# Optimization experiments

Measured on AMD Instinct MI355X. Metric: run time of the kernel, lower is better.

Reference implementation:

```python
import jax, jax.numpy as jnp
import numpy as np

B, H, W, C = 16, 128, 128, 256
C8 = C // 8


def setup_inputs() -> dict:
    key = jax.random.key(0)
    ks = jax.random.split(key, 7)
    s = 0.02
    return {
        "x": jax.random.normal(ks[0], (B, H, W, C), dtype=jnp.float32),
        "wq": jax.random.normal(ks[1], (C, C8), dtype=jnp.float32) * s,
        "bq": jnp.zeros((C8,), dtype=jnp.float32),
        "wk": jax.random.normal(ks[2], (C, C8), dtype=jnp.float32) * s,
        "bk": jnp.zeros((C8,), dtype=jnp.float32),
        "wv": jax.random.normal(ks[3], (C, C), dtype=jnp.float32) * s,
        "bv": jnp.zeros((C,), dtype=jnp.float32),
    }


def reference(x, wq, bq, wk, bk, wv, bv):
    # 1x1 convs == per-pixel linear projections
    q = jnp.einsum("bhwc,cd->bhwd", x, wq) + bq  # [B,H,W,C/8]
    k = jnp.einsum("bhwc,cd->bhwd", x, wk) + bk  # [B,H,W,C/8]
    v = jnp.einsum("bhwc,cd->bhwd", x, wv) + bv  # [B,H,W,C]
    # tf.matmul on 4D: batch over (B,H), attention over W (row-wise)
    scores = jnp.einsum("bhwd,bhvd->bhwv", q, k)  # [B,H,W,W]
    attn = jax.nn.softmax(scores, axis=-1)
    out = jnp.einsum("bhwv,bhvc->bhwc", attn, v)  # [B,H,W,C]
    return out
```

## Files before the change

### kernel.cpp

```cpp
#include <hip/hip_runtime.h>

typedef __attribute__((ext_vector_type(8))) short short8;
typedef __attribute__((ext_vector_type(16))) float f32x16;
typedef __attribute__((ext_vector_type(4))) float float4v;
typedef __attribute__((ext_vector_type(4))) unsigned short ushort4v;
typedef unsigned short u16;

#define MFMA32(a, b, c) __builtin_amdgcn_mfma_f32_32x32x16_bf16((a), (b), (c), 0, 0, 0)

#define W_ 128
#define C_ 256
#define X_LD 136
#define VT_LD 136
#define QK_LD 40
#define P_LD 136

__device__ __forceinline__ u16 f2bf(float f) {
    unsigned u = __builtin_bit_cast(unsigned, f);
    u += 0x7fffu + ((u >> 16) & 1u);
    return (u16)(u >> 16);
}

__device__ __forceinline__ f32x16 zero16() {
    f32x16 z;
#pragma unroll
    for (int i = 0; i < 16; ++i) z[i] = 0.f;
    return z;
}

__device__ __forceinline__ void gll16(const u16* g, const u16* l) {
    auto s = (const __attribute__((address_space(1))) unsigned*)((uintptr_t)g);
    auto d = (__attribute__((address_space(3))) unsigned*)((unsigned)(uintptr_t)l);
    __builtin_amdgcn_global_load_lds(s, d, 16, 0, 0);
}

__device__ __forceinline__ void wg_barrier() {
    asm volatile("s_waitcnt lgkmcnt(0)" ::: "memory");
    __builtin_amdgcn_sched_barrier(0);
    __builtin_amdgcn_s_barrier();
}

__global__ __launch_bounds__(256) void prep_pack(const float* __restrict__ wq,
                                                 const float* __restrict__ wk,
                                                 const float* __restrict__ wv,
                                                 u16* __restrict__ pack) {
    int t = blockIdx.x * 256 + threadIdx.x;
    int j = t & 7;
    int l = (t >> 3) & 63;
    int g = t >> 9;
    int f = g % 10;
    int ktg = g / 10;
    int k = ktg * 16 + ((l >> 5) << 3) + j;
    int c = l & 31;
    float w;
    if (f == 0)      w = wq[k * 32 + c];
    else if (f == 1) w = wk[k * 32 + c];
    else             w = wv[k * 256 + (f - 2) * 32 + c];
    pack[t] = f2bf(w);
}

__global__ __launch_bounds__(256, 2) void attn_fused(
        const float* __restrict__ x,
        const u16* __restrict__ pack,
        const float* __restrict__ bq, const float* __restrict__ bk,
        const float* __restrict__ bv,
        float* __restrict__ out) {
    __shared__ u16 uA[17408];
    __shared__ u16 uC[17408];

    const int slice = blockIdx.x;
    const int tid = threadIdx.x;
    const int lane = tid & 63;
    const int wid = tid >> 6;
    const int lm = lane & 31;
    const int l5 = lane >> 5;
    const int rowbase = wid * 32;
    const float* xs = x + (size_t)slice * (W_ * C_);

    const u16* vw0 = pack + (size_t)(2 + wid) * 512 + lane * 8;
    const u16* vw1 = pack + (size_t)(2 + wid + 4) * 512 + lane * 8;

    f32x16 qa = zero16();
    f32x16 ka = zero16();
    f32x16 vac0[4], vac1[4];
#pragma unroll
    for (int nn = 0; nn < 4; ++nn) { vac0[nn] = zero16(); vac1[nn] = zero16(); }

#pragma unroll
    for (int i = 0; i < 4; ++i) {
        int ks = wid * 4 + i;
        const u16* gs = pack + (size_t)ks * 5120 + lane * 8;
        gll16(gs, &uC[(ks * 2 + 0) * 512]);
        gll16(gs + 512, &uC[(ks * 2 + 1) * 512]);
    }

    for (int c = 0; c < 2; ++c) {
        if (c == 1) wg_barrier();
        {
            int r0 = tid >> 5;
            int col = (tid & 31) * 4;
#pragma unroll
            for (int p = 0; p < 16; ++p) {
                int row = p * 8 + r0;
                float4v xv = *reinterpret_cast<const float4v*>(xs + row * C_ + c * 128 + col);
                ushort4v b4;
                b4[0] = f2bf(xv[0]); b4[1] = f2bf(xv[1]);
                b4[2] = f2bf(xv[2]); b4[3] = f2bf(xv[3]);
                *reinterpret_cast<ushort4v*>(&uA[row * X_LD + col]) = b4;
            }
        }
        __syncthreads();

        short8 wf0[4], wf1[4];
        wf0[0] = *reinterpret_cast<const short8*>(vw0 + (size_t)(c * 8 + 0) * 5120);
        wf1[0] = *reinterpret_cast<const short8*>(vw1 + (size_t)(c * 8 + 0) * 5120);
        wf0[1] = *reinterpret_cast<const short8*>(vw0 + (size_t)(c * 8 + 1) * 5120);
        wf1[1] = *reinterpret_cast<const short8*>(vw1 + (size_t)(c * 8 + 1) * 5120);

#pragma unroll
        for (int kt = 0; kt < 8; ++kt) {
            const int ks = c * 8 + kt;
            if (kt < 6) {
                wf0[(kt + 2) & 3] = *reinterpret_cast<const short8*>(vw0 + (size_t)(ks + 2) * 5120);
                wf1[(kt + 2) & 3] = *reinterpret_cast<const short8*>(vw1 + (size_t)(ks + 2) * 5120);
            }
            short8 xf[4];
#pragma unroll
            for (int nn = 0; nn < 4; ++nn)
                xf[nn] = *reinterpret_cast<const short8*>(&uA[(nn * 32 + lm) * X_LD + kt * 16 + l5 * 8]);
            short8 aqk = *reinterpret_cast<const short8*>(&uA[(rowbase + lm) * X_LD + kt * 16 + l5 * 8]);
            short8 bq8 = *reinterpret_cast<const short8*>(&uC[(ks * 2 + 0) * 512 + lane * 8]);
            short8 bk8 = *reinterpret_cast<const short8*>(&uC[(ks * 2 + 1) * 512 + lane * 8]);
            qa = MFMA32(aqk, bq8, qa);
            ka = MFMA32(aqk, bk8, ka);
#pragma unroll
            for (int nn = 0; nn < 4; ++nn) {
                vac0[nn] = MFMA32(wf0[kt & 3], xf[nn], vac0[nn]);
                vac1[nn] = MFMA32(wf1[kt & 3], xf[nn], vac1[nn]);
            }
        }
    }
    wg_barrier();

    {
        float bqv = bq[lm];
        float bkv = bk[lm];
#pragma unroll
        for (int e = 0; e < 16; ++e) {
            int row = rowbase + (e & 3) + 8 * (e >> 2) + 4 * l5;
            uC[row * QK_LD + lm] = f2bf(qa[e] + bqv);
            uC[5120 + row * QK_LD + lm] = f2bf(ka[e] + bkv);
        }
    }
#pragma unroll
    for (int e = 0; e < 16; ++e) {
        int cl = (e & 3) + 8 * (e >> 2) + 4 * l5;
        float bvv = bv[wid * 32 + cl];
#pragma unroll
        for (int nn = 0; nn < 4; ++nn)
            uA[(wid * 32 + cl) * VT_LD + nn * 32 + lm] = f2bf(vac0[nn][e] + bvv);
    }
    wg_barrier();

    f32x16 s[4];
#pragma unroll
    for (int c2 = 0; c2 < 4; ++c2) s[c2] = zero16();
#pragma unroll
    for (int kt = 0; kt < 2; ++kt) {
        short8 aq = *reinterpret_cast<const short8*>(&uC[(rowbase + lm) * QK_LD + kt * 16 + l5 * 8]);
#pragma unroll
        for (int c2 = 0; c2 < 4; ++c2) {
            short8 bkf = *reinterpret_cast<const short8*>(&uC[5120 + (c2 * 32 + lm) * QK_LD + kt * 16 + l5 * 8]);
            s[c2] = MFMA32(aq, bkf, s[c2]);
        }
    }
    wg_barrier();

#pragma unroll
    for (int e = 0; e < 16; ++e) {
        float m = fmaxf(fmaxf(s[0][e], s[1][e]), fmaxf(s[2][e], s[3][e]));
        m = fmaxf(m, __shfl_xor(m, 1));
        m = fmaxf(m, __shfl_xor(m, 2));
        m = fmaxf(m, __shfl_xor(m, 4));
        m = fmaxf(m, __shfl_xor(m, 8));
        m = fmaxf(m, __shfl_xor(m, 16));
        float e0 = __expf(s[0][e] - m);
        float e1 = __expf(s[1][e] - m);
        float e2 = __expf(s[2][e] - m);
        float e3 = __expf(s[3][e] - m);
        float sum = (e0 + e1) + (e2 + e3);
        sum += __shfl_xor(sum, 1);
        sum += __shfl_xor(sum, 2);
        sum += __shfl_xor(sum, 4);
        sum += __shfl_xor(sum, 8);
        sum += __shfl_xor(sum, 16);
        float inv = 1.0f / sum;
        int row = rowbase + (e & 3) + 8 * (e >> 2) + 4 * l5;
        uC[row * P_LD + lm] = f2bf(e0 * inv);
        uC[row * P_LD + 32 + lm] = f2bf(e1 * inv);
        uC[row * P_LD + 64 + lm] = f2bf(e2 * inv);
        uC[row * P_LD + 96 + lm] = f2bf(e3 * inv);
    }

    float* os = out + (size_t)slice * (W_ * C_);

    f32x16 oc[4];
#pragma unroll
    for (int c2 = 0; c2 < 4; ++c2) oc[c2] = zero16();
#pragma unroll
    for (int kt = 0; kt < 8; ++kt) {
        short8 pa = *reinterpret_cast<const short8*>(&uC[(rowbase + lm) * P_LD + kt * 16 + l5 * 8]);
#pragma unroll
        for (int c2 = 0; c2 < 4; ++c2) {
            short8 vb = *reinterpret_cast<const short8*>(&uA[(c2 * 32 + lm) * VT_LD + kt * 16 + l5 * 8]);
            oc[c2] = MFMA32(pa, vb, oc[c2]);
        }
    }
    wg_barrier();

#pragma unroll
    for (int e = 0; e < 16; ++e) {
        int cl = (e & 3) + 8 * (e >> 2) + 4 * l5;
        float bvv = bv[128 + wid * 32 + cl];
#pragma unroll
        for (int nn = 0; nn < 4; ++nn)
            uA[(wid * 32 + cl) * VT_LD + nn * 32 + lm] = f2bf(vac1[nn][e] + bvv);
    }
#pragma unroll
    for (int c2 = 0; c2 < 4; ++c2)
#pragma unroll
        for (int e = 0; e < 16; ++e) {
            int row = rowbase + (e & 3) + 8 * (e >> 2) + 4 * l5;
            os[row * C_ + c2 * 32 + lm] = oc[c2][e];
        }
    wg_barrier();

#pragma unroll
    for (int c2 = 0; c2 < 4; ++c2) oc[c2] = zero16();
#pragma unroll
    for (int kt = 0; kt < 8; ++kt) {
        short8 pa = *reinterpret_cast<const short8*>(&uC[(rowbase + lm) * P_LD + kt * 16 + l5 * 8]);
#pragma unroll
        for (int c2 = 0; c2 < 4; ++c2) {
            short8 vb = *reinterpret_cast<const short8*>(&uA[(c2 * 32 + lm) * VT_LD + kt * 16 + l5 * 8]);
            oc[c2] = MFMA32(pa, vb, oc[c2]);
        }
    }
#pragma unroll
    for (int c2 = 0; c2 < 4; ++c2)
#pragma unroll
        for (int e = 0; e < 16; ++e) {
            int row = rowbase + (e & 3) + 8 * (e >> 2) + 4 * l5;
            os[row * C_ + 128 + c2 * 32 + lm] = oc[c2][e];
        }
}

extern "C" void kernel_launch(void* const* d_in, const int* in_sizes, int n_in,
                              void* d_out, int out_size, void* d_ws, size_t ws_size,
                              hipStream_t stream) {
    const float* x  = (const float*)d_in[0];
    const float* wq = (const float*)d_in[1];
    const float* bq = (const float*)d_in[2];
    const float* wk = (const float*)d_in[3];
    const float* bk = (const float*)d_in[4];
    const float* wv = (const float*)d_in[5];
    const float* bv = (const float*)d_in[6];
    float* out = (float*)d_out;
    u16* pack = (u16*)d_ws;

    prep_pack<<<320, 256, 0, stream>>>(wq, wk, wv, pack);
    attn_fused<<<2048, 256, 0, stream>>>(x, pack, bq, bk, bv, out);
}
```

Baseline: 165.4 us.

## Compute transposed scores to keep softmax probabilities in registers

Scores are now computed as K·Q^T, so each lane holds a whole query row split across two lane halves. Softmax then needs only one cross-half shuffle instead of a five-step butterfly per element. The bf16 probabilities are repacked through lane shuffles directly into MFMA A-operand fragments, which removes the LDS write/read of P and one workgroup barrier. The Q/K projection also reuses an already loaded x fragment instead of a separate LDS load. The cost is higher register pressure from holding eight P fragments across both PV passes, at an occupancy target of two blocks.

```diff
diff --git a/kernel.cpp b/kernel.cpp
--- a/kernel.cpp
+++ b/kernel.cpp
@@ -3,6 +3,7 @@
 typedef __attribute__((ext_vector_type(8))) short short8;
 typedef __attribute__((ext_vector_type(16))) float f32x16;
 typedef __attribute__((ext_vector_type(4))) float float4v;
+typedef __attribute__((ext_vector_type(4))) unsigned u32x4;
 typedef __attribute__((ext_vector_type(4))) unsigned short ushort4v;
 typedef unsigned short u16;
 
@@ -13,7 +14,6 @@
 #define X_LD 136
 #define VT_LD 136
 #define QK_LD 40
-#define P_LD 136
 
 __device__ __forceinline__ u16 f2bf(float f) {
     unsigned u = __builtin_bit_cast(unsigned, f);
@@ -38,6 +38,7 @@
     asm volatile("s_waitcnt lgkmcnt(0)" ::: "memory");
     __builtin_amdgcn_sched_barrier(0);
     __builtin_amdgcn_s_barrier();
+    __builtin_amdgcn_sched_barrier(0);
 }
 
 __global__ __launch_bounds__(256) void prep_pack(const float* __restrict__ wq,
@@ -49,8 +50,8 @@
     int l = (t >> 3) & 63;
     int g = t >> 9;
     int f = g % 10;
-    int ktg = g / 10;
-    int k = ktg * 16 + ((l >> 5) << 3) + j;
+    int ks = g / 10;
+    int k = ks * 16 + ((l >> 5) << 3) + j;
     int c = l & 31;
     float w;
     if (f == 0)      w = wq[k * 32 + c];
@@ -128,7 +129,7 @@
 #pragma unroll
             for (int nn = 0; nn < 4; ++nn)
                 xf[nn] = *reinterpret_cast<const short8*>(&uA[(nn * 32 + lm) * X_LD + kt * 16 + l5 * 8]);
-            short8 aqk = *reinterpret_cast<const short8*>(&uA[(rowbase + lm) * X_LD + kt * 16 + l5 * 8]);
+            short8 aqk = xf[wid];
             short8 bq8 = *reinterpret_cast<const short8*>(&uC[(ks * 2 + 0) * 512 + lane * 8]);
             short8 bk8 = *reinterpret_cast<const short8*>(&uC[(ks * 2 + 1) * 512 + lane * 8]);
             qa = MFMA32(aqk, bq8, qa);
@@ -162,44 +163,58 @@
     }
     wg_barrier();
 
-    f32x16 s[4];
-#pragma unroll
-    for (int c2 = 0; c2 < 4; ++c2) s[c2] = zero16();
-#pragma unroll
-    for (int kt = 0; kt < 2; ++kt) {
-        short8 aq = *reinterpret_cast<const short8*>(&uC[(rowbase + lm) * QK_LD + kt * 16 + l5 * 8]);
+    f32x16 sT[4];
+#pragma unroll
+    for (int c2 = 0; c2 < 4; ++c2) sT[c2] = zero16();
+#pragma unroll
+    for (int ktd = 0; ktd < 2; ++ktd) {
+        short8 qf = *reinterpret_cast<const short8*>(&uC[(rowbase + lm) * QK_LD + ktd * 16 + l5 * 8]);
 #pragma unroll
         for (int c2 = 0; c2 < 4; ++c2) {
-            short8 bkf = *reinterpret_cast<const short8*>(&uC[5120 + (c2 * 32 + lm) * QK_LD + kt * 16 + l5 * 8]);
-            s[c2] = MFMA32(aq, bkf, s[c2]);
-        }
-    }
-    wg_barrier();
-
-#pragma unroll
-    for (int e = 0; e < 16; ++e) {
-        float m = fmaxf(fmaxf(s[0][e], s[1][e]), fmaxf(s[2][e], s[3][e]));
-        m = fmaxf(m, __shfl_xor(m, 1));
-        m = fmaxf(m, __shfl_xor(m, 2));
-        m = fmaxf(m, __shfl_xor(m, 4));
-        m = fmaxf(m, __shfl_xor(m, 8));
-        m = fmaxf(m, __shfl_xor(m, 16));
-        float e0 = __expf(s[0][e] - m);
-        float e1 = __expf(s[1][e] - m);
-        float e2 = __expf(s[2][e] - m);
-        float e3 = __expf(s[3][e] - m);
-        float sum = (e0 + e1) + (e2 + e3);
-        sum += __shfl_xor(sum, 1);
-        sum += __shfl_xor(sum, 2);
-        sum += __shfl_xor(sum, 4);
-        sum += __shfl_xor(sum, 8);
-        sum += __shfl_xor(sum, 16);
-        float inv = 1.0f / sum;
-        int row = rowbase + (e & 3) + 8 * (e >> 2) + 4 * l5;
-        uC[row * P_LD + lm] = f2bf(e0 * inv);
-        uC[row * P_LD + 32 + lm] = f2bf(e1 * inv);
-        uC[row * P_LD + 64 + lm] = f2bf(e2 * inv);
-        uC[row * P_LD + 96 + lm] = f2bf(e3 * inv);
+            short8 kf = *reinterpret_cast<const short8*>(&uC[5120 + (c2 * 32 + lm) * QK_LD + ktd * 16 + l5 * 8]);
+            sT[c2] = MFMA32(kf, qf, sT[c2]);
+        }
+    }
+
+    float m = sT[0][0];
+#pragma unroll
+    for (int c2 = 0; c2 < 4; ++c2)
+#pragma unroll
+        for (int e = 0; e < 16; ++e) m = fmaxf(m, sT[c2][e]);
+    m = fmaxf(m, __shfl_xor(m, 32));
+    float sum = 0.f;
+#pragma unroll
+    for (int c2 = 0; c2 < 4; ++c2)
+#pragma unroll
+        for (int e = 0; e < 16; ++e) {
+            float v = __expf(sT[c2][e] - m);
+            sT[c2][e] = v;
+            sum += v;
+        }
+    sum += __shfl_xor(sum, 32);
+    const float inv = 1.0f / sum;
+
+    short8 pf[8];
+#pragma unroll
+    for (int c2 = 0; c2 < 4; ++c2) {
+        unsigned bpk[8];
+#pragma unroll
+        for (int i = 0; i < 8; ++i)
+            bpk[i] = (unsigned)f2bf(sT[c2][2 * i] * inv) |
+                     ((unsigned)f2bf(sT[c2][2 * i + 1] * inv) << 16);
+#pragma unroll
+        for (int hh = 0; hh < 2; ++hh) {
+            unsigned s0 = l5 ? bpk[4 * hh + 0] : bpk[4 * hh + 2];
+            unsigned s1 = l5 ? bpk[4 * hh + 1] : bpk[4 * hh + 3];
+            unsigned t0 = (unsigned)__shfl_xor((int)s0, 32);
+            unsigned t1 = (unsigned)__shfl_xor((int)s1, 32);
+            union { u32x4 u; short8 s; } fr;
+            fr.u[0] = l5 ? t0 : bpk[4 * hh + 0];
+            fr.u[1] = l5 ? t1 : bpk[4 * hh + 1];
+            fr.u[2] = l5 ? bpk[4 * hh + 2] : t0;
+            fr.u[3] = l5 ? bpk[4 * hh + 3] : t1;
+            pf[2 * c2 + hh] = fr.s;
+        }
     }
 
     float* os = out + (size_t)slice * (W_ * C_);
@@ -208,12 +223,11 @@
 #pragma unroll
     for (int c2 = 0; c2 < 4; ++c2) oc[c2] = zero16();
 #pragma unroll
-    for (int kt = 0; kt < 8; ++kt) {
-        short8 pa = *reinterpret_cast<const short8*>(&uC[(rowbase + lm) * P_LD + kt * 16 + l5 * 8]);
+    for (int kt16 = 0; kt16 < 8; ++kt16) {
 #pragma unroll
         for (int c2 = 0; c2 < 4; ++c2) {
-            short8 vb = *reinterpret_cast<const short8*>(&uA[(c2 * 32 + lm) * VT_LD + kt * 16 + l5 * 8]);
-            oc[c2] = MFMA32(pa, vb, oc[c2]);
+            short8 vb = *reinterpret_cast<const short8*>(&uA[(c2 * 32 + lm) * VT_LD + kt16 * 16 + l5 * 8]);
+            oc[c2] = MFMA32(pf[kt16], vb, oc[c2]);
         }
     }
     wg_barrier();
@@ -238,12 +252,11 @@
 #pragma unroll
     for (int c2 = 0; c2 < 4; ++c2) oc[c2] = zero16();
 #pragma unroll
-    for (int kt = 0; kt < 8; ++kt) {
-        short8 pa = *reinterpret_cast<const short8*>(&uC[(rowbase + lm) * P_LD + kt * 16 + l5 * 8]);
+    for (int kt16 = 0; kt16 < 8; ++kt16) {
 #pragma unroll
         for (int c2 = 0; c2 < 4; ++c2) {
-            short8 vb = *reinterpret_cast<const short8*>(&uA[(c2 * 32 + lm) * VT_LD + kt * 16 + l5 * 8]);
-            oc[c2] = MFMA32(pa, vb, oc[c2]);
+            short8 vb = *reinterpret_cast<const short8*>(&uA[(c2 * 32 + lm) * VT_LD + kt16 * 16 + l5 * 8]);
+            oc[c2] = MFMA32(pf[kt16], vb, oc[c2]);
         }
     }
 #pragma unroll
```

New measurement: 300.9 us. 81.9% more time.
